# Kernel optimization log

Hardware: AMD Instinct MI355X
Metric: run time of the kernel (lower is better)

Reference implementation:

```python
import jax, jax.numpy as jnp
import numpy as np

# ---- static config (mirrors DRR.__init__ kwargs) ----
NX = NY = NZ = 192            # volume dims
H = W = 192                   # detector height/width
SDR = 300.0                   # source-to-rotation-center distance
DELX = DELY = 2.0             # detector pixel pitch (mm)
X0 = Y0 = 0.0                 # detector offsets
SPACING = (1.0, 1.0, 1.0)     # voxel spacing (mm)
BAM = 1.0                     # bone_attenuation_multiplier
B = 2                         # batch (poses)
N_SUB = H * W // 2            # p_subsample = 0.5


def setup_inputs() -> dict:
    key = jax.random.key(0)
    k1, k2, k3, k4 = jax.random.split(key, 4)
    # CT volume in Hounsfield units, spanning air (-1000) to bone (~2000)
    volume = jax.random.uniform(k1, (NX, NY, NZ), jnp.float32, -1000.0, 2000.0)
    rotations = jax.random.normal(k2, (B, 3), jnp.float32)          # Euler ZYX (rad)
    translations = jax.random.normal(k3, (B, 3), jnp.float32) * 10.0  # mm, near isocenter
    # unique subsampled detector pixel indices (Detector.subsamples[-1])
    subsample_idx = jax.random.permutation(k4, H * W)[:N_SUB].astype(jnp.int32)
    return {"volume": volume, "rotations": rotations,
            "translations": translations, "subsample_idx": subsample_idx}


def _rz(t):
    c, s = jnp.cos(t), jnp.sin(t); z = jnp.zeros_like(t); o = jnp.ones_like(t)
    return jnp.stack([jnp.stack([c, -s, z], -1),
                      jnp.stack([s, c, z], -1),
                      jnp.stack([z, z, o], -1)], -2)


def _ry(t):
    c, s = jnp.cos(t), jnp.sin(t); z = jnp.zeros_like(t); o = jnp.ones_like(t)
    return jnp.stack([jnp.stack([c, z, s], -1),
                      jnp.stack([z, o, z], -1),
                      jnp.stack([-s, z, c], -1)], -2)


def _rx(t):
    c, s = jnp.cos(t), jnp.sin(t); z = jnp.zeros_like(t); o = jnp.ones_like(t)
    return jnp.stack([jnp.stack([o, z, z], -1),
                      jnp.stack([z, c, -s], -1),
                      jnp.stack([z, s, c], -1)], -2)


def _density(volume):
    # DRR.__init__: volume.flip([0]); air/soft/bone HU segmentation + normalization
    vol = jnp.flip(volume, 0)
    soft = (vol > -800.0) & (vol <= 350.0)
    soft_min = jnp.min(jnp.where(soft, vol, jnp.inf))
    d = jnp.where(vol <= -800.0, soft_min,
                  jnp.where(vol > 350.0, vol * BAM, vol))
    d = d - jnp.min(d)
    return d / jnp.max(d)


def _canonical_detector():
    # source on +z at SDR, detector plane at -z; pixel grid with pitch delx/dely
    xs = (jnp.arange(W, dtype=jnp.float32) - (W - 1) / 2.0) * DELX + X0
    ys = (jnp.arange(H, dtype=jnp.float32) - (H - 1) / 2.0) * DELY + Y0
    gy, gx = jnp.meshgrid(ys, xs, indexing="ij")
    tgt = jnp.stack([gx.ravel(), gy.ravel(),
                     jnp.full((H * W,), -SDR, jnp.float32)], -1)  # [H*W, 3]
    src = jnp.array([0.0, 0.0, SDR], jnp.float32)
    return src, tgt


def _siddon(density, source, target):
    """Siddon ray-casting. source [B,3], target [B,N,3] -> line integrals [B,N]."""
    dims = density.shape
    sp = jnp.asarray(SPACING, density.dtype)
    src = source[:, None, :]                     # [B,1,3]
    sdd = target - src                           # [B,N,3]
    sdd_safe = jnp.where(sdd == 0, 1e-9, sdd)
    # parametric intersections with all grid planes per axis
    alist = [(jnp.arange(dims[a] + 1, dtype=density.dtype)[None, None, :] * sp[a]
              - src[..., a:a + 1]) / sdd_safe[..., a:a + 1] for a in range(3)]
    a_first = jnp.stack([al[..., 0] for al in alist], -1)    # [B,N,3]
    a_last = jnp.stack([al[..., -1] for al in alist], -1)
    amin = jnp.maximum(jnp.max(jnp.minimum(a_first, a_last), -1), 0.0)[..., None]
    amax = jnp.minimum(jnp.min(jnp.maximum(a_first, a_last), -1), 1.0)[..., None]
    amax = jnp.maximum(amax, amin)               # ray misses -> zero-length segments
    alphas = jnp.sort(jnp.clip(jnp.concatenate(alist, -1), amin, amax), -1)  # [B,N,M+1]
    mid = 0.5 * (alphas[..., 1:] + alphas[..., :-1])                         # [B,N,M]
    ray_len = jnp.linalg.norm(target - src, axis=-1, keepdims=True)
    step = (alphas[..., 1:] - alphas[..., :-1]) * ray_len                    # [B,N,M]
    pts = src[..., None, :] + mid[..., None] * sdd[..., None, :]             # [B,N,M,3]
    idx = jnp.clip(jnp.floor(pts / sp).astype(jnp.int32), 0,
                   jnp.array(dims, jnp.int32) - 1)
    vox = density[idx[..., 0], idx[..., 1], idx[..., 2]]                     # gather
    return jnp.sum(step * vox, -1)


def reference(volume, rotations, translations, subsample_idx):
    density = _density(volume)
    src_c, tgt_c = _canonical_detector()
    tgt_c = tgt_c[subsample_idx]                                  # [N,3] subsampled rays
    R = _rz(rotations[:, 0]) @ _ry(rotations[:, 1]) @ _rx(rotations[:, 2])  # [B,3,3]
    center = jnp.array([NX, NY, NZ], jnp.float32) * jnp.asarray(SPACING, jnp.float32) / 2.0
    t = translations + center                                     # pose about isocenter
    source = jnp.einsum("bij,j->bi", R, src_c) + t                # [B,3]
    target = jnp.einsum("bij,nj->bni", R, tgt_c) + t[:, None, :]  # [B,N,3]
    img = _siddon(density, source, target)                        # [B,N]
    # reshape_subsampled_drr: scatter into zeros [B, H*W] then view [B,1,H,W]
    drr = jnp.zeros((img.shape[0], H * W), img.dtype).at[:, subsample_idx].set(img)
    return drr.reshape(-1, 1, H, W)
```

## Files before the change

### kernel.cpp

```cpp
#include <hip/hip_runtime.h>
#include <float.h>
#include <math.h>


#define NDIM   192
#define HW     (NDIM * NDIM)
#define NSUB   (HW / 2)
#define NTILE  576
#define NBATCH 2
#define NCHUNK 16
#define NVOX   (NDIM * NDIM * NDIM)
#define SDRF   300.0f
#define RBLK   1728

#define WS_MARK_OFF 16
#define WS_LIST_OFF (16 + HW)
#define WS_CNT_OFF  (WS_LIST_OFF + 4 * NSUB)
#define WS_OFF_OFF  (WS_CNT_OFF + 4 * NTILE)
#define WS_PART_OFF (WS_OFF_OFF + 4 * NTILE)

__global__ __launch_bounds__(256) void reduce_kernel(
    const float* __restrict__ vol, float* __restrict__ parts) {
    const int tid = blockIdx.x * 256 + threadIdx.x;
    const float4* __restrict__ v4 = (const float4*)vol;
    const int S = RBLK * 256;

    float4 r0 = v4[tid + 0 * S];
    float4 r1 = v4[tid + 1 * S];
    float4 r2 = v4[tid + 2 * S];
    float4 r3 = v4[tid + 3 * S];

    float smin = FLT_MAX, rmin = FLT_MAX, rmax = -FLT_MAX;
    float4 rr[4] = {r0, r1, r2, r3};
#pragma unroll
    for (int k = 0; k < 4; ++k) {
        float xs[4] = {rr[k].x, rr[k].y, rr[k].z, rr[k].w};
#pragma unroll
        for (int j = 0; j < 4; ++j) {
            float x = xs[j];
            bool in = (x > -800.0f);
            rmin = fminf(rmin, in ? x : FLT_MAX);
            rmax = fmaxf(rmax, in ? x : -FLT_MAX);
            smin = fminf(smin, (in && x <= 350.0f) ? x : FLT_MAX);
        }
    }
#pragma unroll
    for (int off = 32; off > 0; off >>= 1) {
        smin = fminf(smin, __shfl_down(smin, off));
        rmin = fminf(rmin, __shfl_down(rmin, off));
        rmax = fmaxf(rmax, __shfl_down(rmax, off));
    }
    __shared__ float sm[4], rm[4], rx[4];
    int w = threadIdx.x >> 6;
    if ((threadIdx.x & 63) == 0) { sm[w] = smin; rm[w] = rmin; rx[w] = rmax; }
    __syncthreads();
    if (threadIdx.x == 0) {
        parts[blockIdx.x] =
            fminf(fminf(sm[0], sm[1]), fminf(sm[2], sm[3]));
        parts[RBLK + blockIdx.x] =
            fminf(fminf(rm[0], rm[1]), fminf(rm[2], rm[3]));
        parts[2 * RBLK + blockIdx.x] =
            fmaxf(fmaxf(rx[0], rx[1]), fmaxf(rx[2], rx[3]));
    }
}

__global__ __launch_bounds__(256) void reduce_final(
    const float* __restrict__ parts, float* __restrict__ ws) {
    float smin = FLT_MAX, rmin = FLT_MAX, rmax = -FLT_MAX;
    for (int i = threadIdx.x; i < RBLK; i += 256) {
        smin = fminf(smin, parts[i]);
        rmin = fminf(rmin, parts[RBLK + i]);
        rmax = fmaxf(rmax, parts[2 * RBLK + i]);
    }
#pragma unroll
    for (int off = 32; off > 0; off >>= 1) {
        smin = fminf(smin, __shfl_down(smin, off));
        rmin = fminf(rmin, __shfl_down(rmin, off));
        rmax = fmaxf(rmax, __shfl_down(rmax, off));
    }
    __shared__ float sm[4], rm[4], rx[4];
    int w = threadIdx.x >> 6;
    if ((threadIdx.x & 63) == 0) { sm[w] = smin; rm[w] = rmin; rx[w] = rmax; }
    __syncthreads();
    if (threadIdx.x == 0) {
        ws[0] = fminf(fminf(sm[0], sm[1]), fminf(sm[2], sm[3]));
        ws[1] = fminf(fminf(rm[0], rm[1]), fminf(rm[2], rm[3]));
        ws[2] = fmaxf(fmaxf(rx[0], rx[1]), fmaxf(rx[2], rx[3]));
    }
}

__global__ __launch_bounds__(256) void scatter_mark(
    const int* __restrict__ idx, unsigned char* __restrict__ mark) {
    int n = blockIdx.x * blockDim.x + threadIdx.x;
    if (n < NSUB) mark[idx[n]] = 1;
}

__device__ __forceinline__ int key_to_pixel(int tile, int lane) {
    int pi = (tile / 24) * 8 + (lane >> 3);
    int pj = (tile % 24) * 8 + (lane & 7);
    return pi * NDIM + pj;
}

__global__ __launch_bounds__(256) void count_kernel(
    const unsigned char* __restrict__ mark, int* __restrict__ counts) {
    int lane = threadIdx.x & 63;
    int tile = blockIdx.x * 4 + (threadIdx.x >> 6);
    int p = key_to_pixel(tile, lane);
    unsigned long long mask = __ballot(mark[p] != 0);
    if (lane == 0) counts[tile] = __popcll(mask);
}

__global__ __launch_bounds__(NTILE) void scan_kernel(
    const int* __restrict__ counts, int* __restrict__ offs) {
    __shared__ int s[NTILE];
    int t = threadIdx.x;
    int c = counts[t];
    s[t] = c;
    __syncthreads();
    for (int off = 1; off < NTILE; off <<= 1) {
        int v = s[t];
        int u = (t >= off) ? s[t - off] : 0;
        __syncthreads();
        s[t] = v + u;
        __syncthreads();
    }
    offs[t] = s[t] - c;
}

__global__ __launch_bounds__(256) void emit_kernel(
    const unsigned char* __restrict__ mark, const int* __restrict__ offs,
    int* __restrict__ list) {
    int lane = threadIdx.x & 63;
    int tile = blockIdx.x * 4 + (threadIdx.x >> 6);
    int p = key_to_pixel(tile, lane);
    bool m = (mark[p] != 0);
    unsigned long long mask = __ballot(m);
    int rank = __popcll(mask & ((1ull << lane) - 1ull));
    if (m) list[offs[tile] + rank] = p;
}

__device__ __forceinline__ void init_axis(float s, float d, float a_lo,
                                          int& i, int& st, float& na) {
    if (d > 0.0f) {
        st = 1;
        float f = s + a_lo * d;
        int ii = (int)floorf(f) + 1;
        ii = max(0, min(ii, NDIM + 1));
        while (ii <= NDIM && ((float)ii - s) / d <= a_lo) ++ii;
        while (ii > 0 && ((float)(ii - 1) - s) / d > a_lo) --ii;
        i  = ii;
        na = (ii <= NDIM) ? ((float)ii - s) / d : FLT_MAX;
    } else {
        st = -1;
        float f = s + a_lo * d;
        int ii = (int)ceilf(f) - 1;
        ii = max(-1, min(ii, NDIM));
        while (ii >= 0 && ((float)ii - s) / d <= a_lo) --ii;
        while (ii < NDIM && ((float)(ii + 1) - s) / d > a_lo) ++ii;
        i  = ii;
        na = (ii >= 0) ? ((float)ii - s) / d : FLT_MAX;
    }
}

__global__ __launch_bounds__(256) void ray_kernel(
    const float* __restrict__ vol, const float* __restrict__ rot,
    const float* __restrict__ trans, const float* __restrict__ wsc,
    const int* __restrict__ list, float* __restrict__ out) {
    const int n = blockIdx.x * 256 + threadIdx.x;
    const int c = blockIdx.y;
    const int b = blockIdx.z;

    const int p  = list[n];
    const int pi = p / NDIM;
    const int pj = p % NDIM;

    float smin = wsc[0];
    float rmin = wsc[1];
    float rmax = wsc[2];
    float dmin = fminf(smin, rmin);
    float dmax = fmaxf(smin, rmax);
    float scale = 1.0f / (dmax - dmin);

    float rz = rot[b * 3 + 0], ry = rot[b * 3 + 1], rx = rot[b * 3 + 2];
    float cz = cosf(rz), sz = sinf(rz);
    float cy = cosf(ry), sy = sinf(ry);
    float cx = cosf(rx), sx = sinf(rx);
    float R00 = cz * cy;
    float R01 = cz * sy * sx - sz * cx;
    float R02 = sz * sx + cz * sy * cx;
    float R10 = sz * cy;
    float R11 = cz * cx + sz * sy * sx;
    float R12 = sz * sy * cx - cz * sx;
    float R20 = -sy;
    float R21 = cy * sx;
    float R22 = cy * cx;
    float tx = trans[b * 3 + 0] + 96.0f;
    float ty = trans[b * 3 + 1] + 96.0f;
    float tz = trans[b * 3 + 2] + 96.0f;

    float srcx = R02 * SDRF + tx;
    float srcy = R12 * SDRF + ty;
    float srcz = R22 * SDRF + tz;
    float gx = ((float)pj - 95.5f) * 2.0f;
    float gy = ((float)pi - 95.5f) * 2.0f;
    float tgx = R00 * gx + R01 * gy + R02 * (-SDRF) + tx;
    float tgy = R10 * gx + R11 * gy + R12 * (-SDRF) + ty;
    float tgz = R20 * gx + R21 * gy + R22 * (-SDRF) + tz;

    float sdx = tgx - srcx, sdy = tgy - srcy, sdz = tgz - srcz;
    float dsx = (sdx == 0.0f) ? 1e-9f : sdx;
    float dsy = (sdy == 0.0f) ? 1e-9f : sdy;
    float dsz = (sdz == 0.0f) ? 1e-9f : sdz;

    float af0 = (0.0f - srcx) / dsx, al0 = (192.0f - srcx) / dsx;
    float af1 = (0.0f - srcy) / dsy, al1 = (192.0f - srcy) / dsy;
    float af2 = (0.0f - srcz) / dsz, al2 = (192.0f - srcz) / dsz;
    float amin = fmaxf(fmaxf(fminf(af0, al0), fminf(af1, al1)), fminf(af2, al2));
    amin = fmaxf(amin, 0.0f);
    float amax = fminf(fminf(fmaxf(af0, al0), fmaxf(af1, al1)), fmaxf(af2, al2));
    amax = fminf(amax, 1.0f);
    amax = fmaxf(amax, amin);
    float ray_len = sqrtf(sdx * sdx + sdy * sdy + sdz * sdz);

    float span = amax - amin;
    float a_lo = amin + span * ((float)c / (float)NCHUNK);
    float a_hi = (c == NCHUNK - 1) ? amax
                                   : amin + span * ((float)(c + 1) / (float)NCHUNK);

    int i0, i1, i2, st0, st1, st2;
    float na0, na1, na2;
    init_axis(srcx, dsx, a_lo, i0, st0, na0);
    init_axis(srcy, dsy, a_lo, i1, st1, na1);
    init_axis(srcz, dsz, a_lo, i2, st2, na2);

    float r0 = 1.0f / dsx, r1 = 1.0f / dsy, r2 = 1.0f / dsz;
    float fi0 = (float)i0, fi1 = (float)i1, fi2 = (float)i2;
    float fs0 = (float)st0, fs1 = (float)st1, fs2 = (float)st2;

    float cur = a_lo;
    float acc = 0.0f;
    while (true) {
        float an  = fminf(fminf(na0, na1), na2);
        bool fin  = !(an < a_hi);
        float a2  = fin ? a_hi : an;
        float mid = 0.5f * (cur + a2);
        float px = fmaf(mid, sdx, srcx);
        float py = fmaf(mid, sdy, srcy);
        float pz = fmaf(mid, sdz, srcz);
        int ix = min(max((int)px, 0), NDIM - 1);
        int iy = min(max((int)py, 0), NDIM - 1);
        int iz = min(max((int)pz, 0), NDIM - 1);
        int addr = (NDIM - 1) * HW - ix * HW + iy * NDIM + iz;
        float v  = vol[addr];
        float dv = (v <= -800.0f) ? smin : v;
        acc = fmaf(a2 - cur, dv, acc);
        if (fin) break;
        cur = a2;
        bool c0 = (na0 == an), c1 = (na1 == an), c2 = (na2 == an);
        float nf0 = fi0 + fs0, nf1 = fi1 + fs1, nf2 = fi2 + fs2;
        float nn0 = (nf0 - srcx) * r0;
        float nn1 = (nf1 - srcy) * r1;
        float nn2 = (nf2 - srcz) * r2;
        fi0 = c0 ? nf0 : fi0;  na0 = c0 ? nn0 : na0;
        fi1 = c1 ? nf1 : fi1;  na1 = c1 ? nn1 : na1;
        fi2 = c2 ? nf2 : fi2;  na2 = c2 ? nn2 : na2;
    }
    float res = (acc - dmin * (a_hi - a_lo)) * scale * ray_len;
    atomicAdd(&out[b * HW + p], res);
}

extern "C" void kernel_launch(void* const* d_in, const int* in_sizes, int n_in,
                              void* d_out, int out_size, void* d_ws,
                              size_t ws_size, hipStream_t stream) {
    const float* vol   = (const float*)d_in[0];
    const float* rot   = (const float*)d_in[1];
    const float* trans = (const float*)d_in[2];
    const int*   sidx  = (const int*)d_in[3];
    float* out = (float*)d_out;

    float*         wsf    = (float*)d_ws;
    unsigned char* mark   = (unsigned char*)d_ws + WS_MARK_OFF;
    int*           list   = (int*)((unsigned char*)d_ws + WS_LIST_OFF);
    int*           counts = (int*)((unsigned char*)d_ws + WS_CNT_OFF);
    int*           offs   = (int*)((unsigned char*)d_ws + WS_OFF_OFF);
    float*         parts  = (float*)((unsigned char*)d_ws + WS_PART_OFF);

    hipMemsetAsync(d_out, 0, (size_t)out_size * sizeof(float), stream);
    hipMemsetAsync(mark, 0, HW, stream);

    reduce_kernel<<<RBLK, 256, 0, stream>>>(vol, parts);
    reduce_final<<<1, 256, 0, stream>>>(parts, wsf);
    scatter_mark<<<NSUB / 256, 256, 0, stream>>>(sidx, mark);
    count_kernel<<<NTILE / 4, 256, 0, stream>>>(mark, counts);
    scan_kernel<<<1, NTILE, 0, stream>>>(counts, offs);
    emit_kernel<<<NTILE / 4, 256, 0, stream>>>(mark, offs, list);
    dim3 rgrid(NSUB / 256, NCHUNK, NBATCH);
    ray_kernel<<<rgrid, 256, 0, stream>>>(vol, rot, trans, wsf, list, out);
}
```

Measured before the change: 126.9 us.

## Fuse mark/count/scan/emit setup into a single-block LDS kernel

Replaces the reduce_final, scatter_mark, count, scan and emit kernels and the mark memset with one 1024-thread block. That block builds the pixel mark bitmap in shared memory, counts and scans per tile, and writes the compacted ray list. This cuts five launches and a memset, which matter at this small scale. In exchange the setup work is serialized on one CU, with per-thread sequential emit loops over 64 pixels. The ray loop is also reshaped so the loop-exit test moves to the while condition and the accumulate follows the next-boundary update, to help overlap the gather latency.

Measured after the change: 131.5 us. +3.6%, slower.

```diff
diff --git a/kernel.cpp b/kernel.cpp
--- a/kernel.cpp
+++ b/kernel.cpp
@@ -13,11 +13,8 @@
 #define SDRF   300.0f
 #define RBLK   1728
 
-#define WS_MARK_OFF 16
-#define WS_LIST_OFF (16 + HW)
-#define WS_CNT_OFF  (WS_LIST_OFF + 4 * NSUB)
-#define WS_OFF_OFF  (WS_CNT_OFF + 4 * NTILE)
-#define WS_PART_OFF (WS_OFF_OFF + 4 * NTILE)
+#define WS_LIST_OFF 16
+#define WS_PART_OFF (WS_LIST_OFF + 4 * NSUB)
 
 __global__ __launch_bounds__(256) void reduce_kernel(
     const float* __restrict__ vol, float* __restrict__ parts) {
@@ -64,10 +61,25 @@
     }
 }
 
-__global__ __launch_bounds__(256) void reduce_final(
-    const float* __restrict__ parts, float* __restrict__ ws) {
+__device__ __forceinline__ int key_to_pixel(int tile, int lane) {
+    int pi = (tile / 24) * 8 + (lane >> 3);
+    int pj = (tile % 24) * 8 + (lane & 7);
+    return pi * NDIM + pj;
+}
+
+__global__ __launch_bounds__(1024) void setup_kernel(
+    const float* __restrict__ parts, const int* __restrict__ sidx,
+    float* __restrict__ wsf, int* __restrict__ list) {
+    __shared__ unsigned char smark[HW];
+    __shared__ int s[NTILE];
+    __shared__ float sm[16], rm[16], rx[16];
+    const int t = threadIdx.x;
+
+    int4* sm4 = (int4*)smark;
+    for (int i = t; i < HW / 16; i += 1024) sm4[i] = make_int4(0, 0, 0, 0);
+
     float smin = FLT_MAX, rmin = FLT_MAX, rmax = -FLT_MAX;
-    for (int i = threadIdx.x; i < RBLK; i += 256) {
+    for (int i = t; i < RBLK; i += 1024) {
         smin = fminf(smin, parts[i]);
         rmin = fminf(rmin, parts[RBLK + i]);
         rmax = fmaxf(rmax, parts[2 * RBLK + i]);
@@ -78,65 +90,46 @@
         rmin = fminf(rmin, __shfl_down(rmin, off));
         rmax = fmaxf(rmax, __shfl_down(rmax, off));
     }
-    __shared__ float sm[4], rm[4], rx[4];
-    int w = threadIdx.x >> 6;
-    if ((threadIdx.x & 63) == 0) { sm[w] = smin; rm[w] = rmin; rx[w] = rmax; }
-    __syncthreads();
-    if (threadIdx.x == 0) {
-        ws[0] = fminf(fminf(sm[0], sm[1]), fminf(sm[2], sm[3]));
-        ws[1] = fminf(fminf(rm[0], rm[1]), fminf(rm[2], rm[3]));
-        ws[2] = fmaxf(fmaxf(rx[0], rx[1]), fmaxf(rx[2], rx[3]));
-    }
-}
-
-__global__ __launch_bounds__(256) void scatter_mark(
-    const int* __restrict__ idx, unsigned char* __restrict__ mark) {
-    int n = blockIdx.x * blockDim.x + threadIdx.x;
-    if (n < NSUB) mark[idx[n]] = 1;
-}
-
-__device__ __forceinline__ int key_to_pixel(int tile, int lane) {
-    int pi = (tile / 24) * 8 + (lane >> 3);
-    int pj = (tile % 24) * 8 + (lane & 7);
-    return pi * NDIM + pj;
-}
-
-__global__ __launch_bounds__(256) void count_kernel(
-    const unsigned char* __restrict__ mark, int* __restrict__ counts) {
-    int lane = threadIdx.x & 63;
-    int tile = blockIdx.x * 4 + (threadIdx.x >> 6);
-    int p = key_to_pixel(tile, lane);
-    unsigned long long mask = __ballot(mark[p] != 0);
-    if (lane == 0) counts[tile] = __popcll(mask);
-}
-
-__global__ __launch_bounds__(NTILE) void scan_kernel(
-    const int* __restrict__ counts, int* __restrict__ offs) {
-    __shared__ int s[NTILE];
-    int t = threadIdx.x;
-    int c = counts[t];
-    s[t] = c;
+    int w = t >> 6;
+    if ((t & 63) == 0) { sm[w] = smin; rm[w] = rmin; rx[w] = rmax; }
+    __syncthreads();
+
+    for (int i = t; i < NSUB; i += 1024) smark[sidx[i]] = 1;
+    if (t == 0) {
+        float a = FLT_MAX, b = FLT_MAX, c = -FLT_MAX;
+#pragma unroll
+        for (int k = 0; k < 16; ++k) {
+            a = fminf(a, sm[k]); b = fminf(b, rm[k]); c = fmaxf(c, rx[k]);
+        }
+        wsf[0] = a; wsf[1] = b; wsf[2] = c;
+    }
+    __syncthreads();
+
+    int cnt = 0;
+    if (t < NTILE) {
+#pragma unroll 8
+        for (int lane = 0; lane < 64; ++lane)
+            cnt += smark[key_to_pixel(t, lane)];
+        s[t] = cnt;
+    }
     __syncthreads();
     for (int off = 1; off < NTILE; off <<= 1) {
-        int v = s[t];
-        int u = (t >= off) ? s[t - off] : 0;
+        int v = 0, u = 0;
+        if (t < NTILE) {
+            v = s[t];
+            u = (t >= off) ? s[t - off] : 0;
+        }
         __syncthreads();
-        s[t] = v + u;
+        if (t < NTILE) s[t] = v + u;
         __syncthreads();
     }
-    offs[t] = s[t] - c;
-}
-
-__global__ __launch_bounds__(256) void emit_kernel(
-    const unsigned char* __restrict__ mark, const int* __restrict__ offs,
-    int* __restrict__ list) {
-    int lane = threadIdx.x & 63;
-    int tile = blockIdx.x * 4 + (threadIdx.x >> 6);
-    int p = key_to_pixel(tile, lane);
-    bool m = (mark[p] != 0);
-    unsigned long long mask = __ballot(m);
-    int rank = __popcll(mask & ((1ull << lane) - 1ull));
-    if (m) list[offs[tile] + rank] = p;
+    if (t < NTILE) {
+        int pos = s[t] - cnt;
+        for (int lane = 0; lane < 64; ++lane) {
+            int p = key_to_pixel(t, lane);
+            if (smark[p]) list[pos++] = p;
+        }
+    }
 }
 
 __device__ __forceinline__ void init_axis(float s, float d, float a_lo,
@@ -239,9 +232,10 @@
 
     float cur = a_lo;
     float acc = 0.0f;
-    while (true) {
+    bool fin = false;
+    while (!fin) {
         float an  = fminf(fminf(na0, na1), na2);
-        bool fin  = !(an < a_hi);
+        fin = !(an < a_hi);
         float a2  = fin ? a_hi : an;
         float mid = 0.5f * (cur + a2);
         float px = fmaf(mid, sdx, srcx);
@@ -252,10 +246,6 @@
         int iz = min(max((int)pz, 0), NDIM - 1);
         int addr = (NDIM - 1) * HW - ix * HW + iy * NDIM + iz;
         float v  = vol[addr];
-        float dv = (v <= -800.0f) ? smin : v;
-        acc = fmaf(a2 - cur, dv, acc);
-        if (fin) break;
-        cur = a2;
         bool c0 = (na0 == an), c1 = (na1 == an), c2 = (na2 == an);
         float nf0 = fi0 + fs0, nf1 = fi1 + fs1, nf2 = fi2 + fs2;
         float nn0 = (nf0 - srcx) * r0;
@@ -264,6 +254,9 @@
         fi0 = c0 ? nf0 : fi0;  na0 = c0 ? nn0 : na0;
         fi1 = c1 ? nf1 : fi1;  na1 = c1 ? nn1 : na1;
         fi2 = c2 ? nf2 : fi2;  na2 = c2 ? nn2 : na2;
+        float dv = (v <= -800.0f) ? smin : v;
+        acc = fmaf(a2 - cur, dv, acc);
+        cur = a2;
     }
     float res = (acc - dmin * (a_hi - a_lo)) * scale * ray_len;
     atomicAdd(&out[b * HW + p], res);
@@ -278,22 +271,13 @@
     const int*   sidx  = (const int*)d_in[3];
     float* out = (float*)d_out;
 
-    float*         wsf    = (float*)d_ws;
-    unsigned char* mark   = (unsigned char*)d_ws + WS_MARK_OFF;
-    int*           list   = (int*)((unsigned char*)d_ws + WS_LIST_OFF);
-    int*           counts = (int*)((unsigned char*)d_ws + WS_CNT_OFF);
-    int*           offs   = (int*)((unsigned char*)d_ws + WS_OFF_OFF);
-    float*         parts  = (float*)((unsigned char*)d_ws + WS_PART_OFF);
+    float* wsf   = (float*)d_ws;
+    int*   list  = (int*)((unsigned char*)d_ws + WS_LIST_OFF);
+    float* parts = (float*)((unsigned char*)d_ws + WS_PART_OFF);
 
     hipMemsetAsync(d_out, 0, (size_t)out_size * sizeof(float), stream);
-    hipMemsetAsync(mark, 0, HW, stream);
-
     reduce_kernel<<<RBLK, 256, 0, stream>>>(vol, parts);
-    reduce_final<<<1, 256, 0, stream>>>(parts, wsf);
-    scatter_mark<<<NSUB / 256, 256, 0, stream>>>(sidx, mark);
-    count_kernel<<<NTILE / 4, 256, 0, stream>>>(mark, counts);
-    scan_kernel<<<1, NTILE, 0, stream>>>(counts, offs);
-    emit_kernel<<<NTILE / 4, 256, 0, stream>>>(mark, offs, list);
+    setup_kernel<<<1, 1024, 0, stream>>>(parts, sidx, wsf, list);
     dim3 rgrid(NSUB / 256, NCHUNK, NBATCH);
     ray_kernel<<<rgrid, 256, 0, stream>>>(vol, rot, trans, wsf, list, out);
 }
```
